# Performance work log

Measured on AMD Instinct MI355X. Metric: run time of the kernel, lower is better.

## Reference

```python
import jax, jax.numpy as jnp
import numpy as np

SEQ, B, H = 2048, 2, 4096
N_HEADS = 32
N_KV = 2
HEAD_DIM = H // N_HEADS          # 128
ROT_DIM = HEAD_DIM // 2          # 64 (rope cache last-2 dim = 32 pairs)


def setup_inputs() -> dict:
    key = jax.random.key(0)
    ks = jax.random.split(key, 8)
    hidden_states = jax.random.normal(ks[0], (SEQ, B, H), dtype=jnp.float32)
    rotary_pos_emb = jax.random.normal(ks[1], (SEQ, 1, ROT_DIM // 2, 2), dtype=jnp.float32)
    s = 0.02
    Wq = jax.random.normal(ks[2], (H, H), dtype=jnp.float32) * s
    bq = jnp.zeros((H,), dtype=jnp.float32)
    Wk = jax.random.normal(ks[3], (H, N_KV * HEAD_DIM), dtype=jnp.float32) * s
    bk = jnp.zeros((N_KV * HEAD_DIM,), dtype=jnp.float32)
    Wv = jax.random.normal(ks[4], (H, N_KV * HEAD_DIM), dtype=jnp.float32) * s
    bv = jnp.zeros((N_KV * HEAD_DIM,), dtype=jnp.float32)
    Wo = jax.random.normal(ks[5], (H, H), dtype=jnp.float32) * s
    return {"hidden_states": hidden_states, "rotary_pos_emb": rotary_pos_emb,
            "Wq": Wq, "bq": bq, "Wk": Wk, "bk": bk, "Wv": Wv, "bv": bv, "Wo": Wo}


def _apply_rope(x, rope):
    # x: [sq, b, np, hn]; rope: [sq, 1, rot/2, 2]
    sq = x.shape[0]
    rot = rope.shape[-2] * 2
    x_rot, x_pass = x[..., :rot], x[..., rot:]
    xs = x_rot.reshape(x.shape[0], x.shape[1], x.shape[2], rot // 2, 2)
    rc = rope[:sq].reshape(sq, -1, 1, rot // 2, 2)  # [sq,1,1,rot/2,2]
    o0 = xs[..., 0] * rc[..., 0] - xs[..., 1] * rc[..., 1]
    o1 = xs[..., 1] * rc[..., 0] + xs[..., 0] * rc[..., 1]
    out = jnp.stack([o0, o1], axis=-1).reshape(x_rot.shape)
    return jnp.concatenate([out, x_pass], axis=-1)


def reference(hidden_states, rotary_pos_emb, Wq, bq, Wk, bk, Wv, bv, Wo):
    sq, b, h = hidden_states.shape
    group = N_HEADS // N_KV

    q = (hidden_states @ Wq + bq).reshape(sq, b, N_HEADS, HEAD_DIM)
    k = (hidden_states @ Wk + bk).reshape(sq, b, N_KV, HEAD_DIM)
    v = (hidden_states @ Wv + bv).reshape(sq, b, N_KV, HEAD_DIM)

    q = _apply_rope(q, rotary_pos_emb)
    k = _apply_rope(k, rotary_pos_emb)

    # GQA expand: head index = kv_head * group + g (matches expand+view in torch)
    k = jnp.repeat(k, group, axis=2)  # [sq, b, N_HEADS, hd]
    v = jnp.repeat(v, group, axis=2)

    scale = 1.0 / np.sqrt(HEAD_DIM)
    scores = jnp.einsum("sbhd,tbhd->bhst", q, k) * scale  # [b, nh, sq, sq]
    causal = jnp.tril(jnp.ones((sq, sq), dtype=bool))
    scores = jnp.where(causal, scores, jnp.finfo(scores.dtype).min)
    probs = jax.nn.softmax(scores, axis=-1)
    ctx = jnp.einsum("bhst,tbhd->sbhd", probs, v)  # [sq, b, nh, hd]
    ctx = ctx.reshape(sq, b, h)
    return ctx @ Wo
```

## Files before the change

kernel.cpp:

```cpp
#include <hip/hip_runtime.h>
#include <stdint.h>

#define SEQ   2048
#define BATCH 2
#define HD    4096
#define NH    32
#define NKV   2
#define HDIM  128
#define NT    (SEQ*BATCH)
#define KVC   (NKV*HDIM)

typedef short  bf16x8 __attribute__((ext_vector_type(8)));
typedef short  sh4    __attribute__((ext_vector_type(4)));
typedef float  f32x4  __attribute__((ext_vector_type(4)));
typedef float  f32x16 __attribute__((ext_vector_type(16)));

__device__ __forceinline__ float bf2f(unsigned short u){
  union { unsigned int i; float f; } v; v.i = ((unsigned int)u) << 16; return v.f;
}
__device__ __forceinline__ unsigned short f2bf(float f){
  union { float f; unsigned int i; } v; v.f = f;
  unsigned int r = v.i + 0x7FFFu + ((v.i >> 16) & 1u);
  return (unsigned short)(r >> 16);
}
__device__ __forceinline__ unsigned int cvtpk_bf16(float lo, float hi){
  unsigned int r;
  asm("v_cvt_pk_bf16_f32 %0, %1, %2" : "=v"(r) : "v"(lo), "v"(hi));
  return r;
}
__device__ __forceinline__ void plane_swap(unsigned int &a, unsigned int &b){
  asm("v_permlane32_swap_b32 %0, %1" : "+v"(a), "+v"(b));
}
__device__ __forceinline__ bf16x8 mk_pf(float a0f,float a1f,float a2f,float a3f,
                                        float b0f,float b1f,float b2f,float b3f){
  unsigned int a0 = cvtpk_bf16(a0f, a1f);
  unsigned int a1 = cvtpk_bf16(a2f, a3f);
  unsigned int b0 = cvtpk_bf16(b0f, b1f);
  unsigned int b1 = cvtpk_bf16(b2f, b3f);
  plane_swap(a0, b0);
  plane_swap(a1, b1);
  union { unsigned int u[4]; bf16x8 h; } u;
  u.u[0] = a0; u.u[1] = a1; u.u[2] = b0; u.u[3] = b1;
  return u.h;
}

__device__ __forceinline__ void gload_lds16(const void* g, void* lds){
  __builtin_amdgcn_global_load_lds(
      (const __attribute__((address_space(1))) unsigned int*)(size_t)g,
      (__attribute__((address_space(3))) unsigned int*)(unsigned int)(size_t)lds,
      16, 0, 0);
}

__device__ __forceinline__ void BARRIER(){
  __builtin_amdgcn_sched_barrier(0);
  asm volatile("" ::: "memory");
  __builtin_amdgcn_s_barrier();
  asm volatile("" ::: "memory");
  __builtin_amdgcn_sched_barrier(0);
}
#define VMCNT(N) do { asm volatile("s_waitcnt vmcnt(" #N ")" ::: "memory"); \
                      __builtin_amdgcn_sched_barrier(0); } while(0)

__global__ void k_cast(const float* __restrict__ in, unsigned short* __restrict__ out, int n4){
  int i = blockIdx.x * blockDim.x + threadIdx.x;
  if (i >= n4) return;
  float4 v = ((const float4*)in)[i];
  ushort4 o; o.x = f2bf(v.x); o.y = f2bf(v.y); o.z = f2bf(v.z); o.w = f2bf(v.w);
  ((ushort4*)out)[i] = o;
}

__global__ void k_transpose(const float* __restrict__ W, unsigned short* __restrict__ WT,
                            int K, int N){
  __shared__ float t[32][33];
  int n0 = blockIdx.x * 32, k0 = blockIdx.y * 32;
  int tx = threadIdx.x, ty = threadIdx.y;
  t[ty][tx] = W[(size_t)(k0 + ty) * N + n0 + tx];
  __syncthreads();
  WT[(size_t)(n0 + ty) * K + k0 + tx] = f2bf(t[tx][ty]);
}

template<bool OUTF32>
__global__ __launch_bounds__(256) void k_gemm(
    const unsigned short* __restrict__ A,
    const unsigned short* __restrict__ BT,
    const float* __restrict__ bias,
    const float* __restrict__ bias2, int bsplit,
    void* __restrict__ C, int M, int N, int K)
{
  __shared__ unsigned short As[128*32];
  __shared__ unsigned short Bs[128*32];
  const int tid  = threadIdx.x;
  const int lane = tid & 63;
  const int w    = tid >> 6;
  const int l4   = lane >> 4, l15 = lane & 15;
  const int wm   = (w >> 1) * 64, wn = (w & 1) * 64;
  const size_t bm = (size_t)blockIdx.y * 128, bn = (size_t)blockIdx.x * 128;

  f32x4 acc[4][4] = {};
  const int scol = (lane & 3) * 8;

  for (int k0 = 0; k0 < K; k0 += 32) {
    #pragma unroll
    for (int j = 0; j < 2; ++j) {
      const int r = w*32 + j*16 + (lane >> 2);
      gload_lds16(A  + (bm + r) * (size_t)K + k0 + scol, As + (size_t)(w*32 + j*16) * 32);
      gload_lds16(BT + (bn + r) * (size_t)K + k0 + scol, Bs + (size_t)(w*32 + j*16) * 32);
    }
    __syncthreads();
    bf16x8 af[4], bfr[4];
    #pragma unroll
    for (int m = 0; m < 4; ++m)
      af[m] = *(const bf16x8*)(As + (wm + m*16 + l15)*32 + l4*8);
    #pragma unroll
    for (int n = 0; n < 4; ++n)
      bfr[n] = *(const bf16x8*)(Bs + (wn + n*16 + l15)*32 + l4*8);
    #pragma unroll
    for (int m = 0; m < 4; ++m)
      #pragma unroll
      for (int n = 0; n < 4; ++n)
        acc[m][n] = __builtin_amdgcn_mfma_f32_16x16x32_bf16(af[m], bfr[n], acc[m][n], 0, 0, 0);
    __syncthreads();
  }

  #pragma unroll
  for (int n = 0; n < 4; ++n) {
    const size_t col = bn + wn + n*16 + l15;
    float badd = 0.0f;
    if (bias) badd = (bias2 && (int)col >= bsplit) ? bias2[col - bsplit] : bias[col];
    #pragma unroll
    for (int m = 0; m < 4; ++m) {
      const size_t row0 = bm + wm + m*16 + l4*4;
      #pragma unroll
      for (int r = 0; r < 4; ++r) {
        float v = acc[m][n][r] + badd;
        if (OUTF32) ((float*)C)[(row0 + r) * (size_t)N + col] = v;
        else ((unsigned short*)C)[(row0 + r) * (size_t)N + col] = f2bf(v);
      }
    }
  }
}

template<int MODE>
__global__ __launch_bounds__(512, 2) void k_gemm256(
    const unsigned short* __restrict__ A,
    const unsigned short* __restrict__ BT,
    const float* __restrict__ bias,
    void* __restrict__ C,
    int M, int N, int K)
{
  __shared__ __attribute__((aligned(16))) unsigned short As[2][16384];
  __shared__ __attribute__((aligned(16))) unsigned short Bs[2][16384];
  const int tid  = threadIdx.x;
  const int lane = tid & 63;
  const int w    = tid >> 6;
  const int c    = lane & 15, g = lane >> 4;
  const int wm   = w >> 2, wn = w & 3;

  const int nwg = (int)(gridDim.x * gridDim.y);
  int bid = (int)(blockIdx.y * gridDim.x + blockIdx.x);
  int bx, by;
  if (gridDim.x == 16 && gridDim.y == 16) {
    const int k = bid & 7, cc = bid >> 3;
    by = (k >> 1) * 4 + (cc >> 3);
    bx = (k & 1) * 8 + (cc & 7);
  } else {
    if ((nwg & 7) == 0) bid = (bid & 7) * (nwg >> 3) + (bid >> 3);
    bx = bid % (int)gridDim.x;
    by = bid / (int)gridDim.x;
  }
  const size_t bm = (size_t)by * 256, bn = (size_t)bx * 256;

  const char* Ab = (const char*)(A  + bm * (size_t)K);
  const char* Bb = (const char*)(BT + bn * (size_t)K);
  const size_t Kb2 = (size_t)K * 2;
  const int cswz = (c & 7) << 4;

  f32x4 acc[8][4] = {};
  bf16x8 af[4][2], bfr[4][2];

#define STAGE_A(bi, h, k0) do { \
    _Pragma("unroll") \
    for (int _j = 0; _j < 2; ++_j) { \
      const int _i = _j*512 + tid; \
      const int _row = (h)*128 + (_i >> 3); \
      const int _ch  = _i & 7; \
      gload_lds16(Ab + (size_t)_row * Kb2 + (size_t)(k0)*2 + ((_ch*16) ^ ((_row & 7) << 4)), \
                  (char*)As[bi] + (h)*16384 + _j*8192 + w*1024); \
    } } while(0)
#define STAGE_B(bi, h, k0) do { \
    _Pragma("unroll") \
    for (int _j = 0; _j < 2; ++_j) { \
      const int _i = _j*512 + tid; \
      const int _row = (h)*128 + (_i >> 3); \
      const int _ch  = _i & 7; \
      gload_lds16(Bb + (size_t)_row * Kb2 + (size_t)(k0)*2 + ((_ch*16) ^ ((_row & 7) << 4)), \
                  (char*)Bs[bi] + (h)*16384 + _j*8192 + w*1024); \
    } } while(0)
#define LDA(bi, mg) do { \
    _Pragma("unroll") \
    for (int _m = 0; _m < 4; ++_m) { \
      const char* _p = (const char*)As[bi] + (size_t)(((mg)*128 + _m*32 + wm*16 + c) * 128); \
      af[_m][0] = *(const bf16x8*)(_p + (( 0 + g*16) ^ cswz)); \
      af[_m][1] = *(const bf16x8*)(_p + ((64 + g*16) ^ cswz)); \
    } } while(0)
#define LDB(bi, ng) do { \
    _Pragma("unroll") \
    for (int _n = 0; _n < 2; ++_n) { \
      const char* _p = (const char*)Bs[bi] + (size_t)((((ng)*2+_n)*64 + wn*16 + c) * 128); \
      bfr[(ng)*2+_n][0] = *(const bf16x8*)(_p + (( 0 + g*16) ^ cswz)); \
      bfr[(ng)*2+_n][1] = *(const bf16x8*)(_p + ((64 + g*16) ^ cswz)); \
    } } while(0)
#define MFMA16(mg, ng) do { \
    __builtin_amdgcn_s_setprio(1); \
    _Pragma("unroll") \
    for (int _m = 0; _m < 4; ++_m) \
      _Pragma("unroll") \
      for (int _n = 0; _n < 2; ++_n) { \
        acc[(mg)*4+_m][(ng)*2+_n] = __builtin_amdgcn_mfma_f32_16x16x32_bf16( \
            af[_m][0], bfr[(ng)*2+_n][0], acc[(mg)*4+_m][(ng)*2+_n], 0, 0, 0); \
        acc[(mg)*4+_m][(ng)*2+_n] = __builtin_amdgcn_mfma_f32_16x16x32_bf16( \
            af[_m][1], bfr[(ng)*2+_n][1], acc[(mg)*4+_m][(ng)*2+_n], 0, 0, 0); \
      } \
    __builtin_amdgcn_s_setprio(0); \
  } while(0)

  STAGE_A(0, 0, 0);
  STAGE_B(0, 0, 0);
  STAGE_B(0, 1, 0);
  STAGE_A(0, 1, 0);
  STAGE_A(1, 0, 64);
  STAGE_B(1, 0, 64);
  VMCNT(8);
  BARRIER();

  const int niter = K >> 7;
  for (int it = 0; it < niter; ++it) {
    const int kb = it*128 + 64;
    int k2 = it*128 + 128; if (k2 >= K) k2 = 0;
    int k3 = it*128 + 192; if (k3 >= K) k3 = 0;
    LDA(0, 0); LDB(0, 0);
    STAGE_A(1, 1, kb);
    BARRIER();
    MFMA16(0, 0);
    VMCNT(6);
    BARRIER();
    LDB(0, 1);
    STAGE_B(1, 1, kb);
    BARRIER();
    MFMA16(0, 1);
    BARRIER();
    LDA(0, 1);
    STAGE_A(0, 0, k2);
    BARRIER();
    MFMA16(1, 0);
    BARRIER();
    STAGE_B(0, 0, k2);
    BARRIER();
    MFMA16(1, 1);
    VMCNT(8);
    BARRIER();
    LDA(1, 0); LDB(1, 0);
    STAGE_A(0, 1, k2);
    BARRIER();
    MFMA16(0, 0);
    VMCNT(6);
    BARRIER();
    LDB(1, 1);
    STAGE_B(0, 1, k2);
    BARRIER();
    MFMA16(0, 1);
    BARRIER();
    LDA(1, 1);
    STAGE_A(1, 0, k3);
    BARRIER();
    MFMA16(1, 0);
    BARRIER();
    STAGE_B(1, 0, k3);
    BARRIER();
    MFMA16(1, 1);
    VMCNT(8);
    BARRIER();
  }

  #pragma unroll
  for (int m = 0; m < 8; ++m) {
    const size_t row0 = bm + m*32 + wm*16 + g*4;
    #pragma unroll
    for (int n = 0; n < 4; ++n) {
      const int col = (int)bn + n*64 + wn*16 + c;
      const float badd = bias ? bias[col] : 0.0f;
      #pragma unroll
      for (int r = 0; r < 4; ++r) {
        float v = acc[m][n][r] + badd;
        if (MODE == 1) ((float*)C)[(row0 + r) * (size_t)N + col] = v;
        else ((unsigned short*)C)[(row0 + r) * (size_t)N + col] = f2bf(v);
      }
    }
  }
#undef STAGE_A
#undef STAGE_B
#undef LDA
#undef LDB
#undef MFMA16
}

__global__ void k_rope(const unsigned short* __restrict__ In, const float* __restrict__ rope,
                       unsigned short* __restrict__ Out, int ldin, int ncols, int nslab,
                       int psh, float sc)
{
  int idx = blockIdx.x * 256 + threadIdx.x;
  int npair = ncols >> 1;
  if (idx >= NT * npair) return;
  int t = idx >> psh, pr = idx & (npair - 1);
  int colp = pr * 2, h = colp >> 7, d = colp & 127;
  int s = t >> 1, b = t & 1;
  float x0 = bf2f(In[(size_t)t * ldin + colp]);
  float x1 = bf2f(In[(size_t)t * ldin + colp + 1]);
  float o0 = x0, o1 = x1;
  if (d < 64) {
    int i2 = d >> 1;
    float cr = rope[((size_t)s * 32 + i2) * 2 + 0];
    float ci = rope[((size_t)s * 32 + i2) * 2 + 1];
    o0 = x0 * cr - x1 * ci;
    o1 = x1 * cr + x0 * ci;
  }
  size_t dst = ((size_t)(b * nslab + h) * SEQ + s) * HDIM + d;
  Out[dst]     = f2bf(o0 * sc);
  Out[dst + 1] = f2bf(o1 * sc);
}

__global__ void k_vt(const unsigned short* __restrict__ In, int ld,
                     unsigned short* __restrict__ Out){
  int idx = blockIdx.x * 256 + threadIdx.x;
  if (idx >= NT * KVC) return;
  int t = idx >> 8, cp = idx & 255;
  int kv = cp >> 7, d = cp & 127;
  int s = t >> 1, b = t & 1;
  Out[((size_t)(b * NKV + kv) * HDIM + d) * SEQ + s] = In[(size_t)t * ld + cp];
}

__global__ __launch_bounds__(256, 2) void k_attn(
    const unsigned short* __restrict__ Q,
    const unsigned short* __restrict__ Kk,
    const unsigned short* __restrict__ Vt,
    unsigned short* __restrict__ Ctx)
{
  const int tid  = threadIdx.x;
  const int lane = tid & 63;
  const int w    = tid >> 6;
  const int l31  = lane & 31;
  const int hi   = lane >> 5;
  const int bh = (int)blockIdx.x;
  const int b = bh >> 5, h = bh & 31;
  const int qb = (int)(gridDim.y - 1 - blockIdx.y);
  const int qw0 = qb * 128 + w * 32;

  const unsigned short* Qb = Q  + ((size_t)(b * NH  + h)        * SEQ + qw0) * HDIM;
  const char* Kb = (const char*)(Kk + ((size_t)(b * NKV + (h >> 4)) * SEQ) * HDIM);
  const char* Vb = (const char*)(Vt + ((size_t)(b * NKV + (h >> 4)) * HDIM) * SEQ);

  __shared__ unsigned short Ks[64*128];
  __shared__ unsigned short Vs[128*64];

  bf16x8 qf[8];
  #pragma unroll
  for (int kk = 0; kk < 8; ++kk)
    qf[kk] = *(const bf16x8*)(Qb + (size_t)l31 * HDIM + kk*16 + hi*8);

  f32x16 of0 = {}, of1 = {}, of2 = {}, of3 = {};
  float mrun = -1e30f, lrun = 0.0f;
  const int qmax = qw0 + 31;
  const int qg   = qw0 + l31;
  const int tblk = qb * 128 + 128;

  const int kr = lane >> 4, kc = lane & 15;
  const int vr = lane >> 3, vc = lane & 7;
  const int rswzK = (l31 & 15) << 4;
  const int rswzV = (l31 & 7) << 4;

  for (int t0 = 0; t0 < tblk; t0 += 64) {
    #pragma unroll
    for (int j = 0; j < 4; ++j) {
      const int r = w*16 + j*4 + kr;
      gload_lds16(Kb + (size_t)(t0 + r) * 256 + ((kc*16) ^ ((r & 15) << 4)),
                  (char*)Ks + (w*16 + j*4) * 256);
    }
    #pragma unroll
    for (int j = 0; j < 4; ++j) {
      const int d = w*32 + j*8 + vr;
      gload_lds16(Vb + (size_t)d * (SEQ*2) + (size_t)t0*2 + ((vc*16) ^ ((d & 7) << 4)),
                  (char*)Vs + (w*32 + j*8) * 128);
    }
    __syncthreads();

    if (t0 <= qmax) {
      f32x16 s0 = {};
      #pragma unroll
      for (int kk = 0; kk < 8; ++kk) {
        bf16x8 kf = *(const bf16x8*)((const char*)Ks + l31*256 + ((kk*32 + hi*16) ^ rswzK));
        s0 = __builtin_amdgcn_mfma_f32_32x32x16_bf16(kf, qf[kk], s0, 0, 0, 0);
      }
      const int qh0 = qg - t0 - 4*hi;
      if (t0 + 31 > qw0) {
        #pragma unroll
        for (int r = 0; r < 16; ++r) {
          const int tc = (r & 3) + 8*(r >> 2);
          if (tc > qh0) s0[r] = -1e30f;
        }
      }
      const bool act1 = (t0 + 32 <= qmax);
      f32x16 s1 = {};
      if (act1) {
        #pragma unroll
        for (int kk = 0; kk < 8; ++kk) {
          bf16x8 kf = *(const bf16x8*)((const char*)Ks + (32 + l31)*256 + ((kk*32 + hi*16) ^ rswzK));
          s1 = __builtin_amdgcn_mfma_f32_32x32x16_bf16(kf, qf[kk], s1, 0, 0, 0);
        }
        if (t0 + 63 > qw0) {
          const int qh1 = qh0 - 32;
          #pragma unroll
          for (int r = 0; r < 16; ++r) {
            const int tc = (r & 3) + 8*(r >> 2);
            if (tc > qh1) s1[r] = -1e30f;
          }
        }
      }
      float mloc = s0[0];
      #pragma unroll
      for (int r = 1; r < 16; ++r) mloc = fmaxf(mloc, s0[r]);
      if (act1) {
        #pragma unroll
        for (int r = 0; r < 16; ++r) mloc = fmaxf(mloc, s1[r]);
      }
      mloc = fmaxf(mloc, __shfl_xor(mloc, 32));
      if (!__all(mloc - mrun <= 8.0f)) {
        const float mn = fmaxf(mrun, mloc);
        const float al = exp2f(mrun - mn);
        mrun = mn;
        lrun *= al;
        of0 *= al; of1 *= al; of2 *= al; of3 *= al;
      }
      float ps = 0.0f;
      float p0[16];
      #pragma unroll
      for (int r = 0; r < 16; ++r) { p0[r] = exp2f(s0[r] - mrun); ps += p0[r]; }
      const bf16x8 pf0 = mk_pf(p0[0],p0[1],p0[2],p0[3],   p0[4],p0[5],p0[6],p0[7]);
      const bf16x8 pf1 = mk_pf(p0[8],p0[9],p0[10],p0[11], p0[12],p0[13],p0[14],p0[15]);
      bf16x8 pf2, pf3;
      if (act1) {
        float p1[16];
        #pragma unroll
        for (int r = 0; r < 16; ++r) { p1[r] = exp2f(s1[r] - mrun); ps += p1[r]; }
        pf2 = mk_pf(p1[0],p1[1],p1[2],p1[3],   p1[4],p1[5],p1[6],p1[7]);
        pf3 = mk_pf(p1[8],p1[9],p1[10],p1[11], p1[12],p1[13],p1[14],p1[15]);
      }
      ps += __shfl_xor(ps, 32);
      lrun += ps;

#define PVDT(ofv, dt) do { \
        const char* _vrow = (const char*)Vs + (size_t)(((dt)*32 + l31) * 128); \
        bf16x8 _v0 = *(const bf16x8*)(_vrow + (( 0 + hi*16) ^ rswzV)); \
        bf16x8 _v1 = *(const bf16x8*)(_vrow + ((32 + hi*16) ^ rswzV)); \
        ofv = __builtin_amdgcn_mfma_f32_32x32x16_bf16(_v0, pf0, ofv, 0, 0, 0); \
        ofv = __builtin_amdgcn_mfma_f32_32x32x16_bf16(_v1, pf1, ofv, 0, 0, 0); \
        if (act1) { \
          bf16x8 _v2 = *(const bf16x8*)(_vrow + ((64 + hi*16) ^ rswzV)); \
          bf16x8 _v3 = *(const bf16x8*)(_vrow + ((96 + hi*16) ^ rswzV)); \
          ofv = __builtin_amdgcn_mfma_f32_32x32x16_bf16(_v2, pf2, ofv, 0, 0, 0); \
          ofv = __builtin_amdgcn_mfma_f32_32x32x16_bf16(_v3, pf3, ofv, 0, 0, 0); \
        } } while(0)
      PVDT(of0, 0);
      PVDT(of1, 1);
      PVDT(of2, 2);
      PVDT(of3, 3);
#undef PVDT
    }
    __syncthreads();
  }

  const float inv = 1.0f / lrun;
  unsigned short* Crow = Ctx + ((size_t)(qg * BATCH + b)) * HD + (size_t)h * HDIM;
#define EPI(ofv, dt) do { \
    _Pragma("unroll") \
    for (int _q = 0; _q < 4; ++_q) { \
      const int _col = (dt)*32 + 8*_q + 4*hi; \
      const unsigned int _w0 = cvtpk_bf16(ofv[4*_q+0]*inv, ofv[4*_q+1]*inv); \
      const unsigned int _w1 = cvtpk_bf16(ofv[4*_q+2]*inv, ofv[4*_q+3]*inv); \
      *(unsigned int*)(Crow + _col)     = _w0; \
      *(unsigned int*)(Crow + _col + 2) = _w1; \
    } } while(0)
  EPI(of0, 0);
  EPI(of1, 1);
  EPI(of2, 2);
  EPI(of3, 3);
#undef EPI
}

extern "C" void kernel_launch(void* const* d_in, const int* in_sizes, int n_in,
                              void* d_out, int out_size, void* d_ws, size_t ws_size,
                              hipStream_t stream)
{
  const float* hs   = (const float*)d_in[0];
  const float* rope = (const float*)d_in[1];
  const float* Wq   = (const float*)d_in[2];
  const float* bq   = (const float*)d_in[3];
  const float* Wk   = (const float*)d_in[4];
  const float* bk   = (const float*)d_in[5];
  const float* Wv   = (const float*)d_in[6];
  const float* bv   = (const float*)d_in[7];
  const float* Wo   = (const float*)d_in[8];

  char* ws = (char*)d_ws;
  const size_t MB = (size_t)1 << 20;
  unsigned short* Xbf  = (unsigned short*)(ws);
  unsigned short* Ctx  = Xbf;
  unsigned short* WqT  = (unsigned short*)(ws + 32*MB);
  unsigned short* WkT  = (unsigned short*)(ws + 64*MB);
  unsigned short* WvT  = (unsigned short*)(ws + 66*MB);
  unsigned short* Qa   = WqT;
  unsigned short* WoT  = (unsigned short*)(ws + 68*MB);
  unsigned short* Qtmp = (unsigned short*)(ws + 100*MB);
  unsigned short* KVt  = (unsigned short*)(ws + 132*MB);
  unsigned short* Ka   = (unsigned short*)(ws + 136*MB);
  unsigned short* VTa  = (unsigned short*)(ws + 138*MB);

  k_cast<<<(NT*HD/4 + 255)/256, 256, 0, stream>>>(hs, Xbf, NT*HD/4);

  dim3 tb(32, 32);
  k_transpose<<<dim3(HD/32,  HD/32), tb, 0, stream>>>(Wq, WqT, HD, HD);
  k_transpose<<<dim3(KVC/32, HD/32), tb, 0, stream>>>(Wk, WkT, HD, KVC);
  k_transpose<<<dim3(KVC/32, HD/32), tb, 0, stream>>>(Wv, WvT, HD, KVC);
  k_transpose<<<dim3(HD/32,  HD/32), tb, 0, stream>>>(Wo, WoT, HD, HD);

  k_gemm256<0><<<dim3(HD/256, NT/256), 512, 0, stream>>>(Xbf, WqT, bq, Qtmp, NT, HD, HD);
  k_gemm<false><<<dim3(512/128, NT/128), 256, 0, stream>>>(Xbf, WkT, bk, bv, 256,
                                                           KVt, NT, 512, HD);

  const float scq = 0.08838834764831845f * 1.4426950408889634f;
  k_rope<<<(NT*(HD/2)  + 255)/256, 256, 0, stream>>>(Qtmp, rope, Qa, HD, HD, NH, 11, scq);
  k_rope<<<(NT*(KVC/2) + 255)/256, 256, 0, stream>>>(KVt, rope, Ka, 512, KVC, NKV, 7, 1.0f);
  k_vt  <<<(NT*KVC     + 255)/256, 256, 0, stream>>>(KVt + 256, 512, VTa);

  k_attn<<<dim3(NH*BATCH, SEQ/128), 256, 0, stream>>>(Qa, Ka, VTa, Ctx);

  k_gemm256<1><<<dim3(HD/256, NT/256), 512, 0, stream>>>(Ctx, WoT, nullptr, d_out, NT, HD, HD);
}
```

Measured before the change: 534.9 us.

## Double-buffer K tiles and overlap V load with QK^T and softmax

The attention kernel now keeps two K tiles in shared memory and prefetches the next K tile while the current one is used. The V tile load is issued first and only waited on (vmcnt 4) after QK^T and softmax finish, so global-to-LDS copies overlap compute instead of stalling at a barrier before every step. This costs an extra 16KB of LDS per block, which may lower occupancy, and adds one more barrier per iteration.

New measurement: 539.9 us. About the same (+0.9%).

```diff
diff --git a/kernel.cpp b/kernel.cpp
--- a/kernel.cpp
+++ b/kernel.cpp
@@ -359,7 +359,7 @@
   const char* Kb = (const char*)(Kk + ((size_t)(b * NKV + (h >> 4)) * SEQ) * HDIM);
   const char* Vb = (const char*)(Vt + ((size_t)(b * NKV + (h >> 4)) * HDIM) * SEQ);
 
-  __shared__ unsigned short Ks[64*128];
+  __shared__ unsigned short Ks[2][64*128];
   __shared__ unsigned short Vs[128*64];
 
   bf16x8 qf[8];
@@ -378,26 +378,42 @@
   const int rswzK = (l31 & 15) << 4;
   const int rswzV = (l31 & 7) << 4;
 
+  #pragma unroll
+  for (int j = 0; j < 4; ++j) {
+    const int r = w*16 + j*4 + kr;
+    gload_lds16(Kb + (size_t)r * 256 + ((kc*16) ^ ((r & 15) << 4)),
+                (char*)Ks[0] + (w*16 + j*4) * 256);
+  }
+  VMCNT(0);
+  BARRIER();
+
+  int cur = 0;
   for (int t0 = 0; t0 < tblk; t0 += 64) {
-    #pragma unroll
-    for (int j = 0; j < 4; ++j) {
-      const int r = w*16 + j*4 + kr;
-      gload_lds16(Kb + (size_t)(t0 + r) * 256 + ((kc*16) ^ ((r & 15) << 4)),
-                  (char*)Ks + (w*16 + j*4) * 256);
-    }
+    const int tn = (t0 + 64 < tblk) ? (t0 + 64) : t0;
+
     #pragma unroll
     for (int j = 0; j < 4; ++j) {
       const int d = w*32 + j*8 + vr;
       gload_lds16(Vb + (size_t)d * (SEQ*2) + (size_t)t0*2 + ((vc*16) ^ ((d & 7) << 4)),
                   (char*)Vs + (w*32 + j*8) * 128);
     }
-    __syncthreads();
-
-    if (t0 <= qmax) {
+    #pragma unroll
+    for (int j = 0; j < 4; ++j) {
+      const int r = w*16 + j*4 + kr;
+      gload_lds16(Kb + (size_t)(tn + r) * 256 + ((kc*16) ^ ((r & 15) << 4)),
+                  (char*)Ks[cur ^ 1] + (w*16 + j*4) * 256);
+    }
+
+    const char* Kcur = (const char*)Ks[cur];
+    const bool active = (t0 <= qmax);
+    const bool act1   = (t0 + 32 <= qmax);
+    bf16x8 pf0, pf1, pf2, pf3;
+
+    if (active) {
       f32x16 s0 = {};
       #pragma unroll
       for (int kk = 0; kk < 8; ++kk) {
-        bf16x8 kf = *(const bf16x8*)((const char*)Ks + l31*256 + ((kk*32 + hi*16) ^ rswzK));
+        bf16x8 kf = *(const bf16x8*)(Kcur + l31*256 + ((kk*32 + hi*16) ^ rswzK));
         s0 = __builtin_amdgcn_mfma_f32_32x32x16_bf16(kf, qf[kk], s0, 0, 0, 0);
       }
       const int qh0 = qg - t0 - 4*hi;
@@ -408,12 +424,11 @@
           if (tc > qh0) s0[r] = -1e30f;
         }
       }
-      const bool act1 = (t0 + 32 <= qmax);
       f32x16 s1 = {};
       if (act1) {
         #pragma unroll
         for (int kk = 0; kk < 8; ++kk) {
-          bf16x8 kf = *(const bf16x8*)((const char*)Ks + (32 + l31)*256 + ((kk*32 + hi*16) ^ rswzK));
+          bf16x8 kf = *(const bf16x8*)(Kcur + (32 + l31)*256 + ((kk*32 + hi*16) ^ rswzK));
           s1 = __builtin_amdgcn_mfma_f32_32x32x16_bf16(kf, qf[kk], s1, 0, 0, 0);
         }
         if (t0 + 63 > qw0) {
@@ -444,9 +459,8 @@
       float p0[16];
       #pragma unroll
       for (int r = 0; r < 16; ++r) { p0[r] = exp2f(s0[r] - mrun); ps += p0[r]; }
-      const bf16x8 pf0 = mk_pf(p0[0],p0[1],p0[2],p0[3],   p0[4],p0[5],p0[6],p0[7]);
-      const bf16x8 pf1 = mk_pf(p0[8],p0[9],p0[10],p0[11], p0[12],p0[13],p0[14],p0[15]);
-      bf16x8 pf2, pf3;
+      pf0 = mk_pf(p0[0],p0[1],p0[2],p0[3],   p0[4],p0[5],p0[6],p0[7]);
+      pf1 = mk_pf(p0[8],p0[9],p0[10],p0[11], p0[12],p0[13],p0[14],p0[15]);
       if (act1) {
         float p1[16];
         #pragma unroll
@@ -456,7 +470,12 @@
       }
       ps += __shfl_xor(ps, 32);
       lrun += ps;
-
+    }
+
+    VMCNT(4);
+    BARRIER();
+
+    if (active) {
 #define PVDT(ofv, dt) do { \
         const char* _vrow = (const char*)Vs + (size_t)(((dt)*32 + l31) * 128); \
         bf16x8 _v0 = *(const bf16x8*)(_vrow + (( 0 + hi*16) ^ rswzV)); \
@@ -475,7 +494,10 @@
       PVDT(of3, 3);
 #undef PVDT
     }
-    __syncthreads();
+
+    VMCNT(0);
+    BARRIER();
+    cur ^= 1;
   }
 
   const float inv = 1.0f / lrun;
```
